# Kernel optimization log

Hardware: AMD Instinct MI355X
Metric: run time of the kernel (lower is better)

Reference implementation:

```python
import jax, jax.numpy as jnp
import numpy as np

B, H, S, D = 2, 16, 2048, 64

def setup_inputs() -> dict:
    key = jax.random.key(0)
    kq, kk, kv = jax.random.split(key, 3)
    q = jax.random.normal(kq, (B, H, S, D), dtype=jnp.float32)
    k = jax.random.normal(kk, (B, H, S, D), dtype=jnp.float32)
    v = jax.random.normal(kv, (B, H, S, D), dtype=jnp.float32)
    mask = jnp.tril(jnp.ones((S, S), dtype=bool))  # causal, broadcast over B,H
    return {"q": q, "k": k, "v": v, "mask": mask}

def reference(q, k, v, mask):
    d_k = q.shape[-1]
    # [..., num_q, num_kv]
    qk = jnp.einsum('bhqd,bhkd->bhqk', q, k) / jnp.sqrt(jnp.asarray(d_k, q.dtype))
    qk = jnp.where(mask, qk, -jnp.inf)
    attn = jax.nn.softmax(qk, axis=-1)
    return jnp.einsum('bhqk,bhkd->bhqd', attn, v)
```

## Files before the change

### kernel.cpp

```cpp
#include <hip/hip_runtime.h>

#define SS 2048
#define DD 64
#define BH 32
#define QSCALE 0.1803368801f
#define BUFS 16896

typedef __attribute__((ext_vector_type(8))) short short8;
typedef __attribute__((ext_vector_type(4))) float floatx4;

__device__ __forceinline__ short f2bf(float x) {
  union { float f; unsigned u; } un; un.f = x;
  unsigned r = (un.u + 0x7FFFu + ((un.u >> 16) & 1u)) >> 16;
  return (short)r;
}
__device__ __forceinline__ short f2bf_fast(float x) {
  union { float f; unsigned u; } un; un.f = x;
  return (short)((un.u + 0x8000u) >> 16);
}
__device__ __forceinline__ float fexp2(float x) {
  return __builtin_amdgcn_exp2f(x);
}
__device__ __forceinline__ void gload16(const short* g, short* l) {
  __builtin_amdgcn_global_load_lds(
      (const __attribute__((address_space(1))) void*)g,
      (__attribute__((address_space(3))) void*)l, 16, 0, 0);
}
#define MFMA __builtin_amdgcn_mfma_f32_16x16x32_bf16

__device__ __forceinline__ int kperm(int c) {
  return (((c >> 2) & 1) << 4) + ((c >> 3) << 2) + (c & 3);
}

__global__ __launch_bounds__(256) void prep_kv(const float* __restrict__ K,
                                               const float* __restrict__ V,
                                               short* __restrict__ Kbf,
                                               short* __restrict__ Vtp) {
  __shared__ short Ts[64][72];
  const int bh = blockIdx.x;
  const int r0 = blockIdx.y * 64;
  const int t  = threadIdx.x;
  {
    const int r = t >> 2, c = (t & 3) * 16;
    const float* g = V + ((size_t)bh * SS + r0 + r) * DD + c;
    floatx4 a = *(const floatx4*)g;
    floatx4 b = *(const floatx4*)(g + 4);
    floatx4 cc = *(const floatx4*)(g + 8);
    floatx4 dd = *(const floatx4*)(g + 12);
    short8 x0, x1;
    x0[0]=f2bf(a[0]); x0[1]=f2bf(a[1]); x0[2]=f2bf(a[2]); x0[3]=f2bf(a[3]);
    x0[4]=f2bf(b[0]); x0[5]=f2bf(b[1]); x0[6]=f2bf(b[2]); x0[7]=f2bf(b[3]);
    x1[0]=f2bf(cc[0]);x1[1]=f2bf(cc[1]);x1[2]=f2bf(cc[2]);x1[3]=f2bf(cc[3]);
    x1[4]=f2bf(dd[0]);x1[5]=f2bf(dd[1]);x1[6]=f2bf(dd[2]);x1[7]=f2bf(dd[3]);
    *(short8*)&Ts[r][c] = x0;
    *(short8*)&Ts[r][c + 8] = x1;
  }
  {
    const size_t i = ((size_t)bh * SS + r0) * DD + (size_t)t * 16;
    floatx4 a = *(const floatx4*)(K + i);
    floatx4 b = *(const floatx4*)(K + i + 4);
    floatx4 cc = *(const floatx4*)(K + i + 8);
    floatx4 dd = *(const floatx4*)(K + i + 12);
    short8 x0, x1;
    x0[0]=f2bf(a[0]); x0[1]=f2bf(a[1]); x0[2]=f2bf(a[2]); x0[3]=f2bf(a[3]);
    x0[4]=f2bf(b[0]); x0[5]=f2bf(b[1]); x0[6]=f2bf(b[2]); x0[7]=f2bf(b[3]);
    x1[0]=f2bf(cc[0]);x1[1]=f2bf(cc[1]);x1[2]=f2bf(cc[2]);x1[3]=f2bf(cc[3]);
    x1[4]=f2bf(dd[0]);x1[5]=f2bf(dd[1]);x1[6]=f2bf(dd[2]);x1[7]=f2bf(dd[3]);
    *(short8*)(Kbf + i) = x0;
    *(short8*)(Kbf + i + 8) = x1;
  }
  __syncthreads();
  {
    const int d = t >> 2, cblk = (t & 3) * 16;
    short8 y0, y1;
    #pragma unroll
    for (int jj = 0; jj < 8; ++jj) {
      const int c0 = cblk + jj, c1 = cblk + 8 + jj;
      y0[jj] = Ts[(c0 & 32) + kperm(c0 & 31)][d];
      y1[jj] = Ts[(c1 & 32) + kperm(c1 & 31)][d];
    }
    const int kt  = (r0 + cblk) >> 5;
    const int kin = cblk & 31;
    short* o = Vtp + (((size_t)bh * 64 + kt) * 64 + d) * 32 + kin;
    *(short8*)o = y0;
    *(short8*)(o + 8) = y1;
  }
}

#define TILE_COMPUTE(JJ, MODE)                                               \
  {                                                                          \
    const short* lb = bufp + (JJ) * 2176;                                    \
    const short* vb = bufp + 8704 + (JJ) * 2048;                             \
    short8 kb00 = *(const short8*)(lb + kroA);                               \
    short8 kb01 = *(const short8*)(lb + kroB);                               \
    short8 kb10 = *(const short8*)(lb + kroA + 1088);                        \
    short8 kb11 = *(const short8*)(lb + kroB + 1088);                        \
    short8 vt0 = *(const short8*)(vb + vro);                                 \
    short8 vt1 = *(const short8*)(vb + vro + 512);                           \
    short8 vt2 = *(const short8*)(vb + vro + 1024);                          \
    short8 vt3 = *(const short8*)(vb + vro + 1536);                          \
    floatx4 t0 = z, t1 = z;                                                  \
    t0 = MFMA(kb00, qa0, t0, 0, 0, 0); t0 = MFMA(kb01, qa1, t0, 0, 0, 0);    \
    t1 = MFMA(kb10, qa0, t1, 0, 0, 0); t1 = MFMA(kb11, qa1, t1, 0, 0, 0);    \
    if ((MODE) == 1) {                                                       \
      _Pragma("unroll")                                                      \
      for (int r = 0; r < 4; ++r) {                                          \
        t0[r] = (quad * 4 + r <= l16) ? t0[r] : -1e30f;                      \
        t1[r] = -1e30f;                                                      \
      }                                                                      \
    } else if ((MODE) == 2) {                                                \
      _Pragma("unroll")                                                      \
      for (int r = 0; r < 4; ++r) {                                          \
        t1[r] = (quad * 4 + r <= l16) ? t1[r] : -1e30f;                      \
      }                                                                      \
    }                                                                        \
    short8 pa;                                                               \
    _Pragma("unroll")                                                        \
    for (int r = 0; r < 4; ++r) {                                            \
      pa[r]     = f2bf_fast(fexp2(t0[r]));                                   \
      pa[4 + r] = f2bf_fast(fexp2(t1[r]));                                   \
    }                                                                        \
    sacc = MFMA(ones, pa, sacc, 0, 0, 0);                                    \
    o0 = MFMA(vt0, pa, o0, 0, 0, 0); o1 = MFMA(vt1, pa, o1, 0, 0, 0);        \
    o2 = MFMA(vt2, pa, o2, 0, 0, 0); o3 = MFMA(vt3, pa, o3, 0, 0, 0);        \
  }

__global__ __launch_bounds__(512, 2) void sdpa_fused(
    const float* __restrict__ Q, const short* __restrict__ Kbf,
    const short* __restrict__ Vtp, float* __restrict__ Og) {
  __shared__ __align__(16) short Sh[2][BUFS];

  const int tid  = threadIdx.x;
  const int w    = tid >> 6;
  const int lane = tid & 63;
  const int quad = lane >> 4;
  const int l16  = lane & 15;

  const int bh = blockIdx.x;
  const int jb = blockIdx.y;

  const size_t base = (size_t)bh * SS * DD;
  const short* kbase = Kbf + base;
  const short* vtb   = Vtp + base;

  const int kso = (lane >> 3) * 64 + (((lane & 7) ^ (lane >> 3)) * 8);
  const int vso = (lane >> 2) * 32 + (((lane & 3) ^ ((lane >> 3) & 3)) * 8);
  const int kroA = (l16 >> 3) * 544 + (l16 & 7) * 64 + ((quad ^ (l16 & 7)) * 8);
  const int kroB = (l16 >> 3) * 544 + (l16 & 7) * 64 + (((quad + 4) ^ (l16 & 7)) * 8);
  const int vro  = l16 * 32 + ((quad ^ ((l16 >> 1) & 3)) * 8);

  const int wt = w >> 1, wc = w & 1;
  const size_t gso = (size_t)wt * 2048 + wc * 1024;
  const int dK = wt * 2176 + wc * 1088;
  const int dV = 8704 + wt * 2048 + wc * 1024;

  short8 ones;
  #pragma unroll
  for (int r = 0; r < 8; ++r) ones[r] = (short)0x3F80;
  const floatx4 z = {0.f, 0.f, 0.f, 0.f};
  const int hw = w >> 1;

  for (int phase = 0; phase < 2; ++phase) {
    const int qt = phase ? jb : (15 - jb);
    const int np = qt + 1;
    const int qA = qt * 128 + w * 16;

    {
      const short* gk = kbase + gso + kso;
      gload16(gk,       &Sh[0][dK]);
      gload16(gk + 512, &Sh[0][dK + 544]);
      const short* gv = vtb + gso + vso;
      gload16(gv,       &Sh[0][dV]);
      gload16(gv + 512, &Sh[0][dV + 512]);
    }

    short8 qa0, qa1;
    {
      const float* ga = Q + base + (size_t)(qA + l16) * DD + quad * 8;
      floatx4 a0 = *(const floatx4*)ga,        a1 = *(const floatx4*)(ga + 4);
      floatx4 a2 = *(const floatx4*)(ga + 32), a3 = *(const floatx4*)(ga + 36);
      #pragma unroll
      for (int r = 0; r < 4; ++r) {
        qa0[r] = f2bf(a0[r] * QSCALE); qa0[4 + r] = f2bf(a1[r] * QSCALE);
        qa1[r] = f2bf(a2[r] * QSCALE); qa1[4 + r] = f2bf(a3[r] * QSCALE);
      }
    }

    floatx4 o0 = z, o1 = z, o2 = z, o3 = z;
    floatx4 sacc = z;

    int nb = 0;
    for (int p = 0; p < np; ++p) {
      __asm__ volatile("s_waitcnt vmcnt(0)" ::: "memory");
      __syncthreads();
      const short* bufp = Sh[nb];

      if (p + 1 < np) {
        {
          const size_t go = (size_t)(p + 1) * 8192 + gso;
          const short* gk = kbase + go + kso;
          gload16(gk,       &Sh[nb ^ 1][dK]);
          gload16(gk + 512, &Sh[nb ^ 1][dK + 544]);
          const short* gv = vtb + go + vso;
          gload16(gv,       &Sh[nb ^ 1][dV]);
          gload16(gv + 512, &Sh[nb ^ 1][dV + 512]);
        }
        TILE_COMPUTE(0, 0)
        TILE_COMPUTE(1, 0)
        TILE_COMPUTE(2, 0)
        TILE_COMPUTE(3, 0)
      } else {
        #pragma unroll
        for (int jj = 0; jj < 4; ++jj) {
          if (jj < hw) {
            TILE_COMPUTE(jj, 0)
          } else if (jj == hw) {
            if (w & 1) { TILE_COMPUTE(jj, 2) }
            else       { TILE_COMPUTE(jj, 1) }
          }
        }
      }
      nb ^= 1;
    }

    const float inv = 1.0f / sacc[0];
    o0 *= inv; o1 *= inv; o2 *= inv; o3 *= inv;
    float* ra = Og + base + (size_t)(qA + l16) * DD + quad * 4;
    *(floatx4*)(ra)      = o0;
    *(floatx4*)(ra + 16) = o1;
    *(floatx4*)(ra + 32) = o2;
    *(floatx4*)(ra + 48) = o3;

    if (phase == 0) __syncthreads();
  }
}

extern "C" void kernel_launch(void* const* d_in, const int* in_sizes, int n_in,
                              void* d_out, int out_size, void* d_ws, size_t ws_size,
                              hipStream_t stream) {
  (void)in_sizes; (void)n_in; (void)out_size; (void)ws_size;
  const float* q = (const float*)d_in[0];
  const float* k = (const float*)d_in[1];
  const float* v = (const float*)d_in[2];
  float* o = (float*)d_out;

  short* Kbf = (short*)d_ws;
  short* Vtp = Kbf + (size_t)BH * SS * DD;

  prep_kv<<<dim3(BH, SS / 64), 256, 0, stream>>>(k, v, Kbf, Vtp);
  sdpa_fused<<<dim3(BH, 8), 512, 0, stream>>>(q, Kbf, Vtp, o);
}
```

Measured before the change: 131.2 us.

## Split each 128-row query tile into two 64-row blocks with 4 warps

The attention kernel now launches twice as many blocks of 256 threads, each covering 64 query rows, with the KV staging tile halved to 64 keys per pipeline step. Shared memory per block drops by half, and the causal diagonal handling is adjusted to per-half tile counts. The goal is finer-grained parallelism and better load balance or occupancy across CUs. The cost is more pipeline iterations with a barrier each, and K/V tiles are loaded redundantly by the two half-blocks.

```diff
diff --git a/kernel.cpp b/kernel.cpp
--- a/kernel.cpp
+++ b/kernel.cpp
@@ -4,7 +4,7 @@
 #define DD 64
 #define BH 32
 #define QSCALE 0.1803368801f
-#define BUFS 16896
+#define BUFS 8448
 
 typedef __attribute__((ext_vector_type(8))) short short8;
 typedef __attribute__((ext_vector_type(4))) float floatx4;
@@ -90,7 +90,7 @@
 #define TILE_COMPUTE(JJ, MODE)                                               \
   {                                                                          \
     const short* lb = bufp + (JJ) * 2176;                                    \
-    const short* vb = bufp + 8704 + (JJ) * 2048;                             \
+    const short* vb = bufp + 4352 + (JJ) * 2048;                             \
     short8 kb00 = *(const short8*)(lb + kroA);                               \
     short8 kb01 = *(const short8*)(lb + kroB);                               \
     short8 kb10 = *(const short8*)(lb + kroA + 1088);                        \
@@ -125,7 +125,7 @@
     o2 = MFMA(vt2, pa, o2, 0, 0, 0); o3 = MFMA(vt3, pa, o3, 0, 0, 0);        \
   }
 
-__global__ __launch_bounds__(512, 2) void sdpa_fused(
+__global__ __launch_bounds__(256, 2) void sdpa_fused(
     const float* __restrict__ Q, const short* __restrict__ Kbf,
     const short* __restrict__ Vtp, float* __restrict__ Og) {
   __shared__ __align__(16) short Sh[2][BUFS];
@@ -137,7 +137,9 @@
   const int l16  = lane & 15;
 
   const int bh = blockIdx.x;
-  const int jb = blockIdx.y;
+  const int y  = blockIdx.y;
+  const int jb = y >> 1;
+  const int h  = y & 1;
 
   const size_t base = (size_t)bh * SS * DD;
   const short* kbase = Kbf + base;
@@ -149,11 +151,6 @@
   const int kroB = (l16 >> 3) * 544 + (l16 & 7) * 64 + (((quad + 4) ^ (l16 & 7)) * 8);
   const int vro  = l16 * 32 + ((quad ^ ((l16 >> 1) & 3)) * 8);
 
-  const int wt = w >> 1, wc = w & 1;
-  const size_t gso = (size_t)wt * 2048 + wc * 1024;
-  const int dK = wt * 2176 + wc * 1088;
-  const int dV = 8704 + wt * 2048 + wc * 1024;
-
   short8 ones;
   #pragma unroll
   for (int r = 0; r < 8; ++r) ones[r] = (short)0x3F80;
@@ -162,16 +159,16 @@
 
   for (int phase = 0; phase < 2; ++phase) {
     const int qt = phase ? jb : (15 - jb);
-    const int np = qt + 1;
-    const int qA = qt * 128 + w * 16;
+    const int np = 2 * qt + 1 + h;
+    const int qA = qt * 128 + h * 64 + w * 16;
 
     {
-      const short* gk = kbase + gso + kso;
-      gload16(gk,       &Sh[0][dK]);
-      gload16(gk + 512, &Sh[0][dK + 544]);
-      const short* gv = vtb + gso + vso;
-      gload16(gv,       &Sh[0][dV]);
-      gload16(gv + 512, &Sh[0][dV + 512]);
+      const short* gk = kbase + w * 512 + kso;
+      gload16(gk,        &Sh[0][w * 544]);
+      gload16(gk + 2048, &Sh[0][2176 + w * 544]);
+      const short* gv = vtb + w * 512 + vso;
+      gload16(gv,        &Sh[0][4352 + w * 512]);
+      gload16(gv + 2048, &Sh[0][6400 + w * 512]);
     }
 
     short8 qa0, qa1;
@@ -197,21 +194,19 @@
 
       if (p + 1 < np) {
         {
-          const size_t go = (size_t)(p + 1) * 8192 + gso;
-          const short* gk = kbase + go + kso;
-          gload16(gk,       &Sh[nb ^ 1][dK]);
-          gload16(gk + 512, &Sh[nb ^ 1][dK + 544]);
-          const short* gv = vtb + go + vso;
-          gload16(gv,       &Sh[nb ^ 1][dV]);
-          gload16(gv + 512, &Sh[nb ^ 1][dV + 512]);
+          const size_t go = (size_t)(p + 1) * 4096;
+          const short* gk = kbase + go + w * 512 + kso;
+          gload16(gk,        &Sh[nb ^ 1][w * 544]);
+          gload16(gk + 2048, &Sh[nb ^ 1][2176 + w * 544]);
+          const short* gv = vtb + go + w * 512 + vso;
+          gload16(gv,        &Sh[nb ^ 1][4352 + w * 512]);
+          gload16(gv + 2048, &Sh[nb ^ 1][6400 + w * 512]);
         }
         TILE_COMPUTE(0, 0)
         TILE_COMPUTE(1, 0)
-        TILE_COMPUTE(2, 0)
-        TILE_COMPUTE(3, 0)
       } else {
         #pragma unroll
-        for (int jj = 0; jj < 4; ++jj) {
+        for (int jj = 0; jj < 2; ++jj) {
           if (jj < hw) {
             TILE_COMPUTE(jj, 0)
           } else if (jj == hw) {
@@ -248,5 +243,5 @@
   short* Vtp = Kbf + (size_t)BH * SS * DD;
 
   prep_kv<<<dim3(BH, SS / 64), 256, 0, stream>>>(k, v, Kbf, Vtp);
-  sdpa_fused<<<dim3(BH, 8), 512, 0, stream>>>(q, Kbf, Vtp, o);
-}
+  sdpa_fused<<<dim3(BH, 16), 256, 0, stream>>>(q, Kbf, Vtp, o);
+}
```

Result: slower. 137.2 us (+4.6%).
